# Kernel optimization log

Hardware: AMD Instinct MI355X
Metric: run time of the kernel (lower is better)

The kernel has to match this reference:

```python
import jax, jax.numpy as jnp
import numpy as np

N = 100000      # nodes
E = 1600000     # edges (avg degree 16)
F_IN = 128      # num_features
H = 64          # hidden_dim
C = 7           # num_classes


def setup_inputs() -> dict:
    key = jax.random.key(0)
    ks = jax.random.split(key, 9)
    x = jax.random.normal(ks[0], (N, F_IN), dtype=jnp.float32)
    edge_index = jax.random.randint(ks[1], (2, E), 0, N, dtype=jnp.int32)
    s1 = 1.0 / np.sqrt(F_IN)
    s2 = 1.0 / np.sqrt(H)
    # SAGEConv1: lin_l applied to aggregated neighbors, lin_r to root
    W1l = jax.random.uniform(ks[2], (F_IN, H), jnp.float32, -s1, s1)
    W1r = jax.random.uniform(ks[3], (F_IN, H), jnp.float32, -s1, s1)
    b1 = jax.random.uniform(ks[4], (H,), jnp.float32, -s1, s1)
    # SAGEConv2
    W2l = jax.random.uniform(ks[5], (H, C), jnp.float32, -s2, s2)
    W2r = jax.random.uniform(ks[6], (H, C), jnp.float32, -s2, s2)
    b2 = jax.random.uniform(ks[7], (C,), jnp.float32, -s2, s2)
    return {"x": x, "edge_index": edge_index, "W1l": W1l, "W1r": W1r,
            "b1": b1, "W2l": W2l, "W2r": W2r, "b2": b2}


def _segment_mean(vals, idx, num_segments):
    # scatter-mean: sum messages per destination node, divide by in-degree
    sums = jax.ops.segment_sum(vals, idx, num_segments=num_segments)
    cnt = jax.ops.segment_sum(jnp.ones(idx.shape, vals.dtype), idx,
                              num_segments=num_segments)
    return sums / jnp.maximum(cnt, 1.0)[:, None]


def reference(x, edge_index, W1l, W1r, b1, W2l, W2r, b2):
    src, dst = edge_index[0], edge_index[1]
    # SAGEConv 1: mean of neighbor (src) features at each dst, plus root term
    agg1 = _segment_mean(x[src], dst, N)              # [N, F_IN]
    h = agg1 @ W1l + x @ W1r + b1                     # [N, H]
    h = jax.nn.relu(h)
    # dropout is inactive in eval mode (deterministic reference)
    # SAGEConv 2
    agg2 = _segment_mean(h[src], dst, N)              # [N, H]
    out = agg2 @ W2l + h @ W2r + b2                   # [N, C]
    return jax.nn.log_softmax(out, axis=1)
```

## Files before the change

kernel.cpp:

```cpp
#include <hip/hip_runtime.h>
#include <cstdint>
#include <cstddef>


#define CAP 64
#define BINSZ 128
#define CH 4096

typedef __attribute__((ext_vector_type(8))) short bf16x8v;
typedef __attribute__((ext_vector_type(4))) float f32x4v;

__device__ __forceinline__ float bf2f(unsigned short u) {
  return __uint_as_float(((unsigned int)u) << 16);
}
__device__ __forceinline__ unsigned short f2bf(float f) {
  unsigned int x = __float_as_uint(f);
  unsigned int r = (x + 0x7fffu + ((x >> 16) & 1u)) >> 16;
  return (unsigned short)r;
}

__global__ __launch_bounds__(256) void k_hist(const int* __restrict__ ei,
                                              int* __restrict__ hist,
                                              const float* __restrict__ W1l,
                                              const float* __restrict__ W1r,
                                              unsigned short* __restrict__ wswz,
                                              int* __restrict__ cursor,
                                              int E, int NB, int NCH) {
  const int t = threadIdx.x;
  if (blockIdx.x >= (unsigned)NCH) {
    if (blockIdx.x == (unsigned)NCH && t == 0) *cursor = 0;
    int idx = (blockIdx.x - NCH) * 256 + t;
    int j = idx & 7;
    int lane = (idx >> 3) & 63;
    int c = (idx >> 9) & 7;
    int t4 = idx >> 12;
    int kk = t4 * 32 + (lane >> 4) * 8 + j;
    int nn = c * 16 + (lane & 15);
    float v = (nn < 64) ? W1l[kk * 64 + nn] : W1r[kk * 64 + (nn - 64)];
    wswz[idx] = f2bf(v);
    return;
  }
  __shared__ int lcnt[1024];
  const int c = blockIdx.x;
  for (int i = t; i < NB; i += 256) lcnt[i] = 0;
  __syncthreads();
  const int base = c * CH;
  const int end = min(base + CH, E);
  for (int e = base + t; e < end; e += 256) {
    int d = ei[E + e];
    atomicAdd(&lcnt[d >> 7], 1);
  }
  __syncthreads();
  for (int i = t; i < NB; i += 256) hist[(size_t)i * NCH + c] = lcnt[i];
}

__global__ __launch_bounds__(256) void k_scan_gemm(
    int* __restrict__ hist, int* __restrict__ tot, int* __restrict__ binbase,
    int* __restrict__ cursor, int NB, int NCH, int nScan,
    const float* __restrict__ x, const unsigned short* __restrict__ wswz,
    const float* __restrict__ b1, unsigned short* __restrict__ xl,
    unsigned short* __restrict__ hroot, int Nn) {
  if (blockIdx.x < (unsigned)nScan) {
    const int lane = threadIdx.x & 63;
    const int bin = blockIdx.x * 4 + (threadIdx.x >> 6);
    if (bin >= NB) return;
    int* h = hist + (size_t)bin * NCH;
    int carry = 0;
    for (int base = 0; base < NCH; base += 64) {
      int i = base + lane;
      int v = (i < NCH) ? h[i] : 0;
      int incl = v;
      #pragma unroll
      for (int d = 1; d < 64; d <<= 1) {
        int t = __shfl_up(incl, d, 64);
        if (lane >= d) incl += t;
      }
      if (i < NCH) h[i] = carry + incl - v;
      carry += __shfl(incl, 63, 64);
    }
    if (lane == 0) {
      tot[bin] = carry;
      binbase[bin] = atomicAdd(cursor, carry);
    }
    return;
  }
  __shared__ unsigned short Bsw[16384];
  const int t = threadIdx.x;
  const int bid = blockIdx.x - nScan;
  {
    const uint4* src = (const uint4*)wswz;
    uint4* dst = (uint4*)Bsw;
    #pragma unroll
    for (int i = 0; i < 8; ++i) dst[t + i * 256] = src[t + i * 256];
  }
  __syncthreads();

  const int lane = t & 63;
  const int wid = t >> 6;
  const int quad = lane >> 4;
  const int m = lane & 15;
  const int rowA = bid * 64 + wid * 16 + m;
  const float* xrow = x + (size_t)min(rowA, Nn - 1) * 128;

  f32x4v acc[8];
  #pragma unroll
  for (int c = 0; c < 8; ++c) acc[c] = (f32x4v){0.f, 0.f, 0.f, 0.f};

  #pragma unroll
  for (int t4 = 0; t4 < 4; ++t4) {
    const int koff = t4 * 32 + quad * 8;
    float4 a0 = *(const float4*)(xrow + koff);
    float4 a1 = *(const float4*)(xrow + koff + 4);
    bf16x8v af;
    af[0] = (short)f2bf(a0.x); af[1] = (short)f2bf(a0.y);
    af[2] = (short)f2bf(a0.z); af[3] = (short)f2bf(a0.w);
    af[4] = (short)f2bf(a1.x); af[5] = (short)f2bf(a1.y);
    af[6] = (short)f2bf(a1.z); af[7] = (short)f2bf(a1.w);
    #pragma unroll
    for (int c = 0; c < 8; ++c) {
      const bf16x8v bf_ = *(const bf16x8v*)&Bsw[(((t4 * 8 + c) * 64 + lane)) << 3];
      acc[c] = __builtin_amdgcn_mfma_f32_16x16x32_bf16(af, bf_, acc[c], 0, 0, 0);
    }
  }

  const int rbase = bid * 64 + wid * 16 + quad * 4;
  #pragma unroll
  for (int c = 0; c < 8; ++c) {
    const int col = c * 16 + m;
    #pragma unroll
    for (int i = 0; i < 4; ++i) {
      const int r = rbase + i;
      if (r < Nn) {
        if (c < 4) xl[(size_t)r * 64 + col] = f2bf(acc[c][i]);
        else       hroot[(size_t)r * 64 + (col - 64)] = f2bf(acc[c][i] + b1[col - 64]);
      }
    }
  }
}

__global__ __launch_bounds__(256) void k_scat(const int* __restrict__ ei,
                                              const int* __restrict__ hist,
                                              const int* __restrict__ binbase,
                                              unsigned int* __restrict__ part,
                                              int E, int NB, int NCH) {
  __shared__ int lcur[1024];
  const int c = blockIdx.x, t = threadIdx.x;
  for (int i = t; i < NB; i += 256)
    lcur[i] = hist[(size_t)i * NCH + c] + binbase[i];
  __syncthreads();
  const int base = c * CH;
  const int end = min(base + CH, E);
  for (int e = base + t; e < end; e += 256) {
    int s = ei[e];
    int d = ei[E + e];
    int bin = d >> 7;
    int pos = atomicAdd(&lcur[bin], 1);
    part[pos] = (unsigned)s | ((unsigned)(d & 127) << 17);
  }
}

__global__ __launch_bounds__(256) void k_bucketB(const int* __restrict__ binbase,
                                                 const int* __restrict__ tot,
                                                 const unsigned int* __restrict__ part,
                                                 int* __restrict__ cnt,
                                                 int* __restrict__ bucket) {
  __shared__ int lbkt[BINSZ * CAP];
  __shared__ int ldeg[BINSZ];
  const int b = blockIdx.x, t = threadIdx.x;
  if (t < BINSZ) ldeg[t] = 0;
  __syncthreads();
  const int e0 = binbase[b], e1 = e0 + tot[b];
  for (int i = e0 + t; i < e1; i += 256) {
    unsigned rec = part[i];
    int loc = rec >> 17;
    int p = atomicAdd(&ldeg[loc], 1);
    if (p < CAP) lbkt[loc * CAP + p] = (int)(rec & 0x1FFFFu);
  }
  __syncthreads();
  if (t < BINSZ) cnt[b * BINSZ + t] = ldeg[t];
  const int4* s4 = (const int4*)lbkt;
  int4* d4 = (int4*)(bucket + (size_t)b * BINSZ * CAP);
  #pragma unroll 2
  for (int i = t; i < BINSZ * CAP / 4; i += 256) d4[i] = s4[i];
}

__global__ __launch_bounds__(256) void k_agg1(
    const int* __restrict__ cnt, const int* __restrict__ bucket,
    const unsigned int* __restrict__ xl32, const unsigned int* __restrict__ hroot32,
    unsigned int* __restrict__ hbuf32, int Nn) {
  const int lane = threadIdx.x & 63;
  const int q = lane & 15;
  const int g = lane >> 4;
  const int nw = gridDim.x * (blockDim.x >> 6);
  int n = blockIdx.x * (blockDim.x >> 6) + (threadIdx.x >> 6);
  if (n >= Nn) return;

  int c  = cnt[n];
  int c1 = cnt[min(n + nw, Nn - 1)];
  int m = c < CAP ? c : CAP;
  int sidx = (lane < m) ? bucket[(size_t)n * CAP + lane] : 0;
  if ((unsigned)sidx >= (unsigned)Nn) sidx = 0;
  uint2 hu = *(const uint2*)(hroot32 + (size_t)n * 32 + 2 * q);

  while (true) {
    const int n1 = n + nw;
    const int n1c = min(n1, Nn - 1);
    const int m1 = c1 < CAP ? c1 : CAP;
    int sidx1 = (lane < m1) ? bucket[(size_t)n1c * CAP + lane] : 0;
    uint2 hu1 = *(const uint2*)(hroot32 + (size_t)n1c * 32 + 2 * q);
    int c2 = cnt[min(n1 + nw, Nn - 1)];

    float a0 = 0.f, a1 = 0.f, a2 = 0.f, a3 = 0.f;
    int i = 0;
    for (; i + 16 <= m; i += 16) {
      int rA = __shfl(sidx, i + g, 64);
      int rB = __shfl(sidx, i + 4 + g, 64);
      int rC = __shfl(sidx, i + 8 + g, 64);
      int rD = __shfl(sidx, i + 12 + g, 64);
      uint2 uA = *(const uint2*)(xl32 + (size_t)rA * 32 + 2 * q);
      uint2 uB = *(const uint2*)(xl32 + (size_t)rB * 32 + 2 * q);
      uint2 uC = *(const uint2*)(xl32 + (size_t)rC * 32 + 2 * q);
      uint2 uD = *(const uint2*)(xl32 + (size_t)rD * 32 + 2 * q);
      a0 += (__uint_as_float(uA.x << 16) + __uint_as_float(uB.x << 16))
          + (__uint_as_float(uC.x << 16) + __uint_as_float(uD.x << 16));
      a1 += (__uint_as_float(uA.x & 0xFFFF0000u) + __uint_as_float(uB.x & 0xFFFF0000u))
          + (__uint_as_float(uC.x & 0xFFFF0000u) + __uint_as_float(uD.x & 0xFFFF0000u));
      a2 += (__uint_as_float(uA.y << 16) + __uint_as_float(uB.y << 16))
          + (__uint_as_float(uC.y << 16) + __uint_as_float(uD.y << 16));
      a3 += (__uint_as_float(uA.y & 0xFFFF0000u) + __uint_as_float(uB.y & 0xFFFF0000u))
          + (__uint_as_float(uC.y & 0xFFFF0000u) + __uint_as_float(uD.y & 0xFFFF0000u));
    }
    for (; i + 8 <= m; i += 8) {
      int rA = __shfl(sidx, i + g, 64);
      int rB = __shfl(sidx, i + 4 + g, 64);
      uint2 uA = *(const uint2*)(xl32 + (size_t)rA * 32 + 2 * q);
      uint2 uB = *(const uint2*)(xl32 + (size_t)rB * 32 + 2 * q);
      a0 += __uint_as_float(uA.x << 16) + __uint_as_float(uB.x << 16);
      a1 += __uint_as_float(uA.x & 0xFFFF0000u) + __uint_as_float(uB.x & 0xFFFF0000u);
      a2 += __uint_as_float(uA.y << 16) + __uint_as_float(uB.y << 16);
      a3 += __uint_as_float(uA.y & 0xFFFF0000u) + __uint_as_float(uB.y & 0xFFFF0000u);
    }
    for (; i < m; i += 4) {
      int e = i + g;
      int r = __shfl(sidx, e & 63, 64);
      uint2 u = *(const uint2*)(xl32 + (size_t)r * 32 + 2 * q);
      if (e < m) {
        a0 += __uint_as_float(u.x << 16);
        a1 += __uint_as_float(u.x & 0xFFFF0000u);
        a2 += __uint_as_float(u.y << 16);
        a3 += __uint_as_float(u.y & 0xFFFF0000u);
      }
    }
    a0 += __shfl_xor(a0, 16, 64); a0 += __shfl_xor(a0, 32, 64);
    a1 += __shfl_xor(a1, 16, 64); a1 += __shfl_xor(a1, 32, 64);
    a2 += __shfl_xor(a2, 16, 64); a2 += __shfl_xor(a2, 32, 64);
    a3 += __shfl_xor(a3, 16, 64); a3 += __shfl_xor(a3, 32, 64);
    if (g == 0) {
      float inv = __builtin_amdgcn_rcpf(c > 0 ? (float)c : 1.f);
      float h0 = fmaxf(fmaf(a0, inv, __uint_as_float(hu.x << 16)), 0.f);
      float h1 = fmaxf(fmaf(a1, inv, __uint_as_float(hu.x & 0xFFFF0000u)), 0.f);
      float h2 = fmaxf(fmaf(a2, inv, __uint_as_float(hu.y << 16)), 0.f);
      float h3 = fmaxf(fmaf(a3, inv, __uint_as_float(hu.y & 0xFFFF0000u)), 0.f);
      uint2 o;
      o.x = (unsigned)f2bf(h0) | ((unsigned)f2bf(h1) << 16);
      o.y = (unsigned)f2bf(h2) | ((unsigned)f2bf(h3) << 16);
      *(uint2*)(hbuf32 + (size_t)n * 32 + 2 * q) = o;
    }
    if (n1 >= Nn) break;
    n = n1; c = c1; c1 = c2; m = m1;
    sidx = ((unsigned)sidx1 >= (unsigned)Nn) ? 0 : sidx1;
    hu = hu1;
  }
}

__global__ __launch_bounds__(128) void k_gemm2(
    const unsigned short* __restrict__ hbuf,
    const float* __restrict__ W2l, const float* __restrict__ W2r,
    const float* __restrict__ b2,
    float* __restrict__ hl, float* __restrict__ hr, int Nn) {
  __shared__ float tile[128 * 65];
  const int t = threadIdx.x;
  const int rowbase = blockIdx.x * 128;
  for (int idx = t; idx < 128 * 64; idx += 128) {
    int r = idx >> 6, k = idx & 63;
    int n = rowbase + r;
    tile[r * 65 + k] = (n < Nn) ? bf2f(hbuf[(size_t)n * 64 + k]) : 0.f;
  }
  __syncthreads();
  int n = rowbase + t;
  if (n >= Nn) return;
  float al[7] = {0, 0, 0, 0, 0, 0, 0};
  float ar[7] = {0, 0, 0, 0, 0, 0, 0};
  for (int k = 0; k < 64; ++k) {
    float hv = tile[t * 65 + k];
    #pragma unroll
    for (int c = 0; c < 7; ++c) {
      al[c] = fmaf(hv, W2l[k * 7 + c], al[c]);
      ar[c] = fmaf(hv, W2r[k * 7 + c], ar[c]);
    }
  }
  #pragma unroll
  for (int c = 0; c < 7; ++c) {
    hl[(size_t)n * 8 + c] = al[c];
    hr[(size_t)n * 8 + c] = ar[c] + b2[c];
  }
  hl[(size_t)n * 8 + 7] = 0.f;
  hr[(size_t)n * 8 + 7] = 0.f;
}

__global__ __launch_bounds__(256) void k_out(
    const int* __restrict__ cnt, const int* __restrict__ bucket,
    const float* __restrict__ hl, const float* __restrict__ hr,
    float* __restrict__ out, int Nn) {
  const int lane = threadIdx.x & 63;
  const int c = lane & 7;
  const int sub = lane >> 3;
  const int gw = blockIdx.x * (blockDim.x >> 6) + (threadIdx.x >> 6);
  const int n = gw * 8 + sub;
  if (n >= Nn) return;
  int cn = cnt[n];
  int m = cn < CAP ? cn : CAP;
  const bool act = (c < 7);
  float acc = 0.f;
  for (int e0 = 0; e0 < m; e0 += 8) {
    int bv = (e0 + c < m) ? bucket[(size_t)n * CAP + e0 + c] : 0;
    #pragma unroll
    for (int cc = 0; cc < 8; ++cc) {
      if (e0 + cc < m) {
        int s = __shfl(bv, (lane & 56) + cc, 64);
        if ((unsigned)s >= (unsigned)Nn) s = 0;
        if (act) acc += hl[(size_t)s * 8 + c];
      }
    }
  }
  float dd = cn > 0 ? (float)cn : 1.f;
  float v = act ? (acc / dd + hr[(size_t)n * 8 + c]) : -INFINITY;
  float mx = v;
  mx = fmaxf(mx, __shfl_xor(mx, 1, 8));
  mx = fmaxf(mx, __shfl_xor(mx, 2, 8));
  mx = fmaxf(mx, __shfl_xor(mx, 4, 8));
  float ex = act ? expf(v - mx) : 0.f;
  float s2 = ex;
  s2 += __shfl_xor(s2, 1, 8);
  s2 += __shfl_xor(s2, 2, 8);
  s2 += __shfl_xor(s2, 4, 8);
  float res = v - mx - logf(s2);
  if (act) out[(size_t)n * 7 + c] = res;
}

static inline size_t alignup(size_t v) { return (v + 255) & ~(size_t)255; }

extern "C" void kernel_launch(void* const* d_in, const int* in_sizes, int n_in,
                              void* d_out, int out_size, void* d_ws, size_t ws_size,
                              hipStream_t stream) {
  const int N = in_sizes[0] / 128;
  const int E = in_sizes[1] / 2;
  const int NB = (N + BINSZ - 1) / BINSZ;
  const int Np = NB * BINSZ;
  const int NCH = (E + CH - 1) / CH;
  const int nScan = (NB + 3) / 4;

  const float* x   = (const float*)d_in[0];
  const int*   ei  = (const int*)d_in[1];
  const float* W1l = (const float*)d_in[2];
  const float* W1r = (const float*)d_in[3];
  const float* b1  = (const float*)d_in[4];
  const float* W2l = (const float*)d_in[5];
  const float* W2r = (const float*)d_in[6];
  const float* b2  = (const float*)d_in[7];
  float* out = (float*)d_out;

  char* p = (char*)d_ws;
  int* hist    = (int*)p;            p += alignup((size_t)NB * NCH * 4);
  int* tot     = (int*)p;            p += alignup((size_t)NB * 4);
  int* binbase = (int*)p;            p += alignup((size_t)(NB + 1) * 4);
  int* cursor  = (int*)p;            p += alignup(4);
  unsigned int* part = (unsigned int*)p; p += alignup((size_t)E * 4);
  int* cnt    = (int*)p;             p += alignup((size_t)Np * 4);
  int* bucket = (int*)p;             p += alignup((size_t)Np * CAP * 4);
  unsigned short* wswz = (unsigned short*)p; p += alignup((size_t)16384 * 2);
  unsigned short* xl    = (unsigned short*)p; p += alignup((size_t)N * 64 * 2);
  unsigned short* hroot = (unsigned short*)p; p += alignup((size_t)N * 64 * 2);
  unsigned short* hbuf  = (unsigned short*)p; p += alignup((size_t)N * 64 * 2);
  float* hl  = (float*)p;            p += alignup((size_t)N * 8 * 4);
  float* hr  = (float*)p;            p += alignup((size_t)N * 8 * 4);

  dim3 b256(256);
  k_hist<<<dim3(NCH + 64), b256, 0, stream>>>(ei, hist, W1l, W1r, wswz, cursor, E, NB, NCH);
  k_scan_gemm<<<dim3(nScan + (N + 63) / 64), b256, 0, stream>>>(
      hist, tot, binbase, cursor, NB, NCH, nScan, x, wswz, b1, xl, hroot, N);
  k_scat<<<dim3(NCH), b256, 0, stream>>>(ei, hist, binbase, part, E, NB, NCH);
  k_bucketB<<<dim3(NB), b256, 0, stream>>>(binbase, tot, part, cnt, bucket);
  k_agg1<<<dim3(2048), b256, 0, stream>>>(cnt, bucket,
      (const unsigned int*)xl, (const unsigned int*)hroot, (unsigned int*)hbuf, N);
  k_gemm2<<<dim3((N + 127) / 128), dim3(128), 0, stream>>>(hbuf, W2l, W2r, b2, hl, hr, N);
  const int waves_out = (N + 7) / 8;
  k_out<<<dim3((waves_out + 3) / 4), b256, 0, stream>>>(cnt, bucket, hl, hr, out, N);
}
```

Before: 248.8 us.

## Fuse layer-2 projection into aggregation kernel and drop hbuf round trip

Folds the layer-2 linear projections (W2l, W2r, b2) into the first aggregation kernel, which now computes h in registers and reduces 16 partial dot products per wave with cross-lane shuffles. The separate gemm2 kernel and the bf16 hidden buffer are removed, saving one launch and a write plus re-read of the hidden activations. Address arithmetic also switches from 64-bit to 32-bit shifts. In exchange each wave does extra shuffle reductions and holds weight registers, which may reduce occupancy, and h is no longer rounded to bf16 before projection.

```diff
diff --git a/kernel.cpp b/kernel.cpp
--- a/kernel.cpp
+++ b/kernel.cpp
@@ -187,27 +187,46 @@
 __global__ __launch_bounds__(256) void k_agg1(
     const int* __restrict__ cnt, const int* __restrict__ bucket,
     const unsigned int* __restrict__ xl32, const unsigned int* __restrict__ hroot32,
-    unsigned int* __restrict__ hbuf32, int Nn) {
+    const float* __restrict__ W2l, const float* __restrict__ W2r,
+    const float* __restrict__ b2,
+    float* __restrict__ hl, float* __restrict__ hr, int Nn) {
   const int lane = threadIdx.x & 63;
   const int q = lane & 15;
+  const unsigned qo = 2u * q;
   const int g = lane >> 4;
   const int nw = gridDim.x * (blockDim.x >> 6);
   int n = blockIdx.x * (blockDim.x >> 6) + (threadIdx.x >> 6);
   if (n >= Nn) return;
 
+  float wreg[4][4];
+  float bcr[4];
+  #pragma unroll
+  for (int k = 0; k < 4; ++k) {
+    const int o = (g << 2) + k;
+    bcr[k] = (o >= 8 && o < 15) ? b2[o - 8] : 0.f;
+    #pragma unroll
+    for (int j = 0; j < 4; ++j) {
+      const int kk = (q << 2) + j;
+      float wv = 0.f;
+      if (o < 7)                 wv = W2l[kk * 7 + o];
+      else if (o >= 8 && o < 15) wv = W2r[kk * 7 + (o - 8)];
+      wreg[j][k] = wv;
+    }
+  }
+
   int c  = cnt[n];
   int c1 = cnt[min(n + nw, Nn - 1)];
   int m = c < CAP ? c : CAP;
-  int sidx = (lane < m) ? bucket[(size_t)n * CAP + lane] : 0;
+  int sidx = (lane < m) ? bucket[((unsigned)n << 6) + lane] : 0;
   if ((unsigned)sidx >= (unsigned)Nn) sidx = 0;
-  uint2 hu = *(const uint2*)(hroot32 + (size_t)n * 32 + 2 * q);
+  uint2 hu = *(const uint2*)(hroot32 + ((unsigned)n << 5) + qo);
 
   while (true) {
     const int n1 = n + nw;
     const int n1c = min(n1, Nn - 1);
     const int m1 = c1 < CAP ? c1 : CAP;
-    int sidx1 = (lane < m1) ? bucket[(size_t)n1c * CAP + lane] : 0;
-    uint2 hu1 = *(const uint2*)(hroot32 + (size_t)n1c * 32 + 2 * q);
+    int sidx1 = (lane < m1) ? bucket[((unsigned)n1c << 6) + lane] : 0;
+    uint2 hu1 = *(const uint2*)(hroot32 + ((unsigned)n1c << 5) + qo);
     int c2 = cnt[min(n1 + nw, Nn - 1)];
 
     float a0 = 0.f, a1 = 0.f, a2 = 0.f, a3 = 0.f;
@@ -217,10 +236,10 @@
       int rB = __shfl(sidx, i + 4 + g, 64);
       int rC = __shfl(sidx, i + 8 + g, 64);
       int rD = __shfl(sidx, i + 12 + g, 64);
-      uint2 uA = *(const uint2*)(xl32 + (size_t)rA * 32 + 2 * q);
-      uint2 uB = *(const uint2*)(xl32 + (size_t)rB * 32 + 2 * q);
-      uint2 uC = *(const uint2*)(xl32 + (size_t)rC * 32 + 2 * q);
-      uint2 uD = *(const uint2*)(xl32 + (size_t)rD * 32 + 2 * q);
+      uint2 uA = *(const uint2*)(xl32 + (((unsigned)rA) << 5) + qo);
+      uint2 uB = *(const uint2*)(xl32 + (((unsigned)rB) << 5) + qo);
+      uint2 uC = *(const uint2*)(xl32 + (((unsigned)rC) << 5) + qo);
+      uint2 uD = *(const uint2*)(xl32 + (((unsigned)rD) << 5) + qo);
       a0 += (__uint_as_float(uA.x << 16) + __uint_as_float(uB.x << 16))
           + (__uint_as_float(uC.x << 16) + __uint_as_float(uD.x << 16));
       a1 += (__uint_as_float(uA.x & 0xFFFF0000u) + __uint_as_float(uB.x & 0xFFFF0000u))
@@ -233,8 +252,8 @@
     for (; i + 8 <= m; i += 8) {
       int rA = __shfl(sidx, i + g, 64);
       int rB = __shfl(sidx, i + 4 + g, 64);
-      uint2 uA = *(const uint2*)(xl32 + (size_t)rA * 32 + 2 * q);
-      uint2 uB = *(const uint2*)(xl32 + (size_t)rB * 32 + 2 * q);
+      uint2 uA = *(const uint2*)(xl32 + (((unsigned)rA) << 5) + qo);
+      uint2 uB = *(const uint2*)(xl32 + (((unsigned)rB) << 5) + qo);
       a0 += __uint_as_float(uA.x << 16) + __uint_as_float(uB.x << 16);
       a1 += __uint_as_float(uA.x & 0xFFFF0000u) + __uint_as_float(uB.x & 0xFFFF0000u);
       a2 += __uint_as_float(uA.y << 16) + __uint_as_float(uB.y << 16);
@@ -243,7 +262,7 @@
     for (; i < m; i += 4) {
       int e = i + g;
       int r = __shfl(sidx, e & 63, 64);
-      uint2 u = *(const uint2*)(xl32 + (size_t)r * 32 + 2 * q);
+      uint2 u = *(const uint2*)(xl32 + (((unsigned)r) << 5) + qo);
       if (e < m) {
         a0 += __uint_as_float(u.x << 16);
         a1 += __uint_as_float(u.x & 0xFFFF0000u);
@@ -255,57 +274,43 @@
     a1 += __shfl_xor(a1, 16, 64); a1 += __shfl_xor(a1, 32, 64);
     a2 += __shfl_xor(a2, 16, 64); a2 += __shfl_xor(a2, 32, 64);
     a3 += __shfl_xor(a3, 16, 64); a3 += __shfl_xor(a3, 32, 64);
-    if (g == 0) {
+
+    {
       float inv = __builtin_amdgcn_rcpf(c > 0 ? (float)c : 1.f);
       float h0 = fmaxf(fmaf(a0, inv, __uint_as_float(hu.x << 16)), 0.f);
       float h1 = fmaxf(fmaf(a1, inv, __uint_as_float(hu.x & 0xFFFF0000u)), 0.f);
       float h2 = fmaxf(fmaf(a2, inv, __uint_as_float(hu.y << 16)), 0.f);
       float h3 = fmaxf(fmaf(a3, inv, __uint_as_float(hu.y & 0xFFFF0000u)), 0.f);
-      uint2 o;
-      o.x = (unsigned)f2bf(h0) | ((unsigned)f2bf(h1) << 16);
-      o.y = (unsigned)f2bf(h2) | ((unsigned)f2bf(h3) << 16);
-      *(uint2*)(hbuf32 + (size_t)n * 32 + 2 * q) = o;
+      float r0 = h0 * wreg[0][0];
+      r0 = fmaf(h1, wreg[1][0], r0); r0 = fmaf(h2, wreg[2][0], r0); r0 = fmaf(h3, wreg[3][0], r0);
+      float r1 = h0 * wreg[0][1];
+      r1 = fmaf(h1, wreg[1][1], r1); r1 = fmaf(h2, wreg[2][1], r1); r1 = fmaf(h3, wreg[3][1], r1);
+      float r2 = h0 * wreg[0][2];
+      r2 = fmaf(h1, wreg[1][2], r2); r2 = fmaf(h2, wreg[2][2], r2); r2 = fmaf(h3, wreg[3][2], r2);
+      float r3 = h0 * wreg[0][3];
+      r3 = fmaf(h1, wreg[1][3], r3); r3 = fmaf(h2, wreg[2][3], r3); r3 = fmaf(h3, wreg[3][3], r3);
+      #pragma unroll
+      for (int d = 1; d < 16; d <<= 1) {
+        r0 += __shfl_xor(r0, d, 64);
+        r1 += __shfl_xor(r1, d, 64);
+        r2 += __shfl_xor(r2, d, 64);
+        r3 += __shfl_xor(r3, d, 64);
+      }
+      r0 += bcr[0]; r1 += bcr[1]; r2 += bcr[2]; r3 += bcr[3];
+      if (q < 4) {
+        float v = r0;
+        if (q == 1) v = r1;
+        else if (q == 2) v = r2;
+        else if (q == 3) v = r3;
+        float* bp = (g < 2) ? hl : hr;
+        bp[((unsigned)n << 3) + ((g & 1) << 2) + q] = v;
+      }
     }
     if (n1 >= Nn) break;
     n = n1; c = c1; c1 = c2; m = m1;
     sidx = ((unsigned)sidx1 >= (unsigned)Nn) ? 0 : sidx1;
     hu = hu1;
   }
-}
-
-__global__ __launch_bounds__(128) void k_gemm2(
-    const unsigned short* __restrict__ hbuf,
-    const float* __restrict__ W2l, const float* __restrict__ W2r,
-    const float* __restrict__ b2,
-    float* __restrict__ hl, float* __restrict__ hr, int Nn) {
-  __shared__ float tile[128 * 65];
-  const int t = threadIdx.x;
-  const int rowbase = blockIdx.x * 128;
-  for (int idx = t; idx < 128 * 64; idx += 128) {
-    int r = idx >> 6, k = idx & 63;
-    int n = rowbase + r;
-    tile[r * 65 + k] = (n < Nn) ? bf2f(hbuf[(size_t)n * 64 + k]) : 0.f;
-  }
-  __syncthreads();
-  int n = rowbase + t;
-  if (n >= Nn) return;
-  float al[7] = {0, 0, 0, 0, 0, 0, 0};
-  float ar[7] = {0, 0, 0, 0, 0, 0, 0};
-  for (int k = 0; k < 64; ++k) {
-    float hv = tile[t * 65 + k];
-    #pragma unroll
-    for (int c = 0; c < 7; ++c) {
-      al[c] = fmaf(hv, W2l[k * 7 + c], al[c]);
-      ar[c] = fmaf(hv, W2r[k * 7 + c], ar[c]);
-    }
-  }
-  #pragma unroll
-  for (int c = 0; c < 7; ++c) {
-    hl[(size_t)n * 8 + c] = al[c];
-    hr[(size_t)n * 8 + c] = ar[c] + b2[c];
-  }
-  hl[(size_t)n * 8 + 7] = 0.f;
-  hr[(size_t)n * 8 + 7] = 0.f;
 }
 
 __global__ __launch_bounds__(256) void k_out(
@@ -381,7 +386,6 @@
   unsigned short* wswz = (unsigned short*)p; p += alignup((size_t)16384 * 2);
   unsigned short* xl    = (unsigned short*)p; p += alignup((size_t)N * 64 * 2);
   unsigned short* hroot = (unsigned short*)p; p += alignup((size_t)N * 64 * 2);
-  unsigned short* hbuf  = (unsigned short*)p; p += alignup((size_t)N * 64 * 2);
   float* hl  = (float*)p;            p += alignup((size_t)N * 8 * 4);
   float* hr  = (float*)p;            p += alignup((size_t)N * 8 * 4);
 
@@ -392,8 +396,8 @@
   k_scat<<<dim3(NCH), b256, 0, stream>>>(ei, hist, binbase, part, E, NB, NCH);
   k_bucketB<<<dim3(NB), b256, 0, stream>>>(binbase, tot, part, cnt, bucket);
   k_agg1<<<dim3(2048), b256, 0, stream>>>(cnt, bucket,
-      (const unsigned int*)xl, (const unsigned int*)hroot, (unsigned int*)hbuf, N);
-  k_gemm2<<<dim3((N + 127) / 128), dim3(128), 0, stream>>>(hbuf, W2l, W2r, b2, hl, hr, N);
+      (const unsigned int*)xl, (const unsigned int*)hroot,
+      W2l, W2r, b2, hl, hr, N);
   const int waves_out = (N + 7) / 8;
   k_out<<<dim3((waves_out + 3) / 4), b256, 0, stream>>>(cnt, bucket, hl, hr, out, N);
 }
```

After: 245.9 us. About the same (-1.2%).
